# Kernel optimization log

Measured on AMD Instinct MI355X. Metric: run time of the kernel, lower is better.

## Reference

```python
import jax, jax.numpy as jnp
import numpy as np

KEYS = 11     # inference_keys: number of heatmap channels / keypoints
NSTACK = 4
B, H, W = 16, 128, 128


def setup_inputs() -> dict:
    key = jax.random.key(0)
    k1, k2, k3 = jax.random.split(key, 3)
    combined_preds = jax.random.normal(k1, (B, NSTACK, 2 * KEYS, H, W), dtype=jnp.float32)
    heatmaps = jax.random.uniform(k2, (B, KEYS, H, W), dtype=jnp.float32)
    # labels[..., 9] and [..., 10] are keypoint coords; scale to [0, 160) so some
    # fall outside [0, H)=[0,128) and exercise the validity-mask branch.
    labels = jax.random.uniform(k3, (B, KEYS, 11), dtype=jnp.float32) * 160.0
    return {"combined_preds": combined_preds, "heatmaps": heatmaps, "labels": labels}


def reference(combined_preds, heatmaps, labels):
    keys = KEYS
    hm = combined_preds[:, :, :keys]          # [B, S, K, H, W] heatmap preds
    lb = combined_preds[:, :, keys:]          # [B, S, K, H, W] label preds
    b, s, k, m, n = hm.shape                  # m = H, n = W (code uses m for both // and %)

    # HeatmapLoss per stack, vectorized over the stack dim
    heat_loss = ((hm - heatmaps[:, None]) ** 2).sum(axis=(2, 3, 4))  # [B, S]

    # LabelLoss, fully vectorized over (B, S, K)
    flat = hm.reshape(b, s, k, m * n)
    index = jnp.argmax(flat, axis=-1)         # [B, S, K]
    x = index // m                            # matches int(index / m) in original
    y = index % m
    # a[x, y] where a is the [H, W] heatmap -> flat[x * W + y]
    a_xy = jnp.take_along_axis(flat, (x * n + y)[..., None], axis=-1)[..., 0]

    pred = lb.reshape(b, s, k, -1)            # [B, S, K, H*W]
    lab = labels[:, None]                     # [B, 1, K, 11] broadcast over stacks

    gx, gy = lab[..., 9], lab[..., 10]
    valid = (gx > 0) & (gy > 0) & (gx < m) & (gy < n)

    xf = x.astype(pred.dtype)
    yf = y.astype(pred.dtype)
    xy_loss = (gx + lab[..., 7] - xf - pred[..., 7]) ** 2 \
            + (gy + lab[..., 8] - yf - pred[..., 8]) ** 2
    conf_loss = (1.0 - a_xy) ** 2
    class_loss = ((pred[..., 0:7] - lab[..., 0:7]) ** 2).sum(axis=-1)

    per_kp = jnp.where(valid, class_loss + xy_loss + conf_loss, 0.0)  # [B, S, K]
    label_loss = per_kp.sum(axis=-1)                                   # [B, S]

    return heat_loss, label_loss
```

## Files before the change

### kernel.cpp

```cpp
#include <hip/hip_runtime.h>
#include <math.h>

#define KEYS 11
#define NSTACK 4
#define NB 16
#define HH 128
#define WW 128
#define HW (HH * WW)

__global__ void kp_zero_out(float* out) {
    out[threadIdx.x] = 0.0f;
}

__global__ __launch_bounds__(256) void kp_loss_kernel(
    const float* __restrict__ cp,
    const float* __restrict__ heat,
    const float* __restrict__ lab,
    float* __restrict__ out)
{
    const int bid = blockIdx.x;
    const int k  = bid % KEYS;
    const int bs = bid / KEYS;
    const int s  = bs % NSTACK;
    const int b  = bs / NSTACK;

    const float* __restrict__ hm = cp + ((size_t)((b * NSTACK + s) * (2 * KEYS) + k)) * HW;
    const float* __restrict__ ht = heat + ((size_t)(b * KEYS + k)) * HW;

    const int tid = threadIdx.x;
    float sum  = 0.0f;
    float vmax = -INFINITY;
    int   imax = 0;

    const float4* __restrict__ hm4 = (const float4*)hm;
    const float4* __restrict__ ht4 = (const float4*)ht;

    #pragma unroll 4
    for (int i = tid; i < HW / 4; i += 256) {
        float4 a = hm4[i];
        float4 c = ht4[i];
        float d0 = a.x - c.x, d1 = a.y - c.y, d2 = a.z - c.z, d3 = a.w - c.w;
        sum += d0 * d0 + d1 * d1 + d2 * d2 + d3 * d3;
        int base = i * 4;
        if (a.x > vmax) { vmax = a.x; imax = base;     }
        if (a.y > vmax) { vmax = a.y; imax = base + 1; }
        if (a.z > vmax) { vmax = a.z; imax = base + 2; }
        if (a.w > vmax) { vmax = a.w; imax = base + 3; }
    }

    #pragma unroll
    for (int off = 32; off > 0; off >>= 1) {
        float ov = __shfl_down(vmax, off);
        int   oi = __shfl_down(imax, off);
        float os = __shfl_down(sum,  off);
        sum += os;
        if (ov > vmax || (ov == vmax && oi < imax)) { vmax = ov; imax = oi; }
    }

    __shared__ float s_sum[4];
    __shared__ float s_v[4];
    __shared__ int   s_i[4];
    const int wave = tid >> 6;
    if ((tid & 63) == 0) { s_sum[wave] = sum; s_v[wave] = vmax; s_i[wave] = imax; }
    __syncthreads();

    if (tid == 0) {
        #pragma unroll
        for (int w = 1; w < 4; w++) {
            sum += s_sum[w];
            if (s_v[w] > vmax || (s_v[w] == vmax && s_i[w] < imax)) {
                vmax = s_v[w]; imax = s_i[w];
            }
        }
        atomicAdd(&out[bs], sum);

        const float* __restrict__ lb = cp + ((size_t)((b * NSTACK + s) * (2 * KEYS) + KEYS + k)) * HW;
        const float* __restrict__ L  = lab + (size_t)(b * KEYS + k) * 11;
        float gx = L[9], gy = L[10];
        bool valid = (gx > 0.0f) && (gy > 0.0f) && (gx < (float)HH) && (gy < (float)WW);
        if (valid) {
            float xf = (float)(imax / WW);
            float yf = (float)(imax % WW);
            float dx = gx + L[7] - xf - lb[7];
            float dy = gy + L[8] - yf - lb[8];
            float loss = dx * dx + dy * dy;
            float cm = 1.0f - vmax;
            loss += cm * cm;
            #pragma unroll
            for (int j = 0; j < 7; j++) {
                float d = lb[j] - L[j];
                loss += d * d;
            }
            atomicAdd(&out[64 + bs], loss);
        }
    }
}

extern "C" void kernel_launch(void* const* d_in, const int* in_sizes, int n_in,
                              void* d_out, int out_size, void* d_ws, size_t ws_size,
                              hipStream_t stream) {
    const float* cp   = (const float*)d_in[0];
    const float* heat = (const float*)d_in[1];
    const float* lab  = (const float*)d_in[2];
    float* out = (float*)d_out;

    kp_zero_out<<<1, 128, 0, stream>>>(out);
    kp_loss_kernel<<<NB * NSTACK * KEYS, 256, 0, stream>>>(cp, heat, lab, out);
}
```

Measured before the change: 135.8 us.

## Split each heatmap slice across four blocks and reduce partials in a final kernel

Each (batch, stack, key) heatmap slice is now processed by four blocks instead of one, each covering a quarter of the pixels. Partial sums and argmax candidates go to workspace, and a single-block final kernel merges them, computes the label loss and writes outputs directly. This replaces the zeroing kernel and atomics and raises block count for more memory-level parallelism. The cost is an extra serial single-block launch with workspace round trips. Argmax tie-breaking still favours the lower chunk because the merge uses a strict greater-than in chunk order.

```diff
diff --git a/kernel.cpp b/kernel.cpp
--- a/kernel.cpp
+++ b/kernel.cpp
@@ -7,39 +7,38 @@
 #define HH 128
 #define WW 128
 #define HW (HH * WW)
+#define CHUNKS 4
+#define CHUNK_F4 1024
+#define NSLICE (NB * NSTACK * KEYS)
+#define NPART (NSLICE * CHUNKS)
 
-__global__ void kp_zero_out(float* out) {
-    out[threadIdx.x] = 0.0f;
-}
 
-__global__ __launch_bounds__(256) void kp_loss_kernel(
+__global__ __launch_bounds__(256) void kp_partial_kernel(
     const float* __restrict__ cp,
     const float* __restrict__ heat,
-    const float* __restrict__ lab,
-    float* __restrict__ out)
+    float* __restrict__ ws)
 {
-    const int bid = blockIdx.x;
-    const int k  = bid % KEYS;
-    const int bs = bid / KEYS;
-    const int s  = bs % NSTACK;
-    const int b  = bs / NSTACK;
+    const int bid   = blockIdx.x;
+    const int c     = bid & 3;
+    const int slice = bid >> 2;
+    const int k  = slice % KEYS;
+    const int bs = slice / KEYS;
+    const int b  = bs >> 2;
 
-    const float* __restrict__ hm = cp + ((size_t)((b * NSTACK + s) * (2 * KEYS) + k)) * HW;
-    const float* __restrict__ ht = heat + ((size_t)(b * KEYS + k)) * HW;
+    const float4* __restrict__ hm4 = (const float4*)(cp + ((size_t)(bs * (2 * KEYS) + k)) * HW);
+    const float4* __restrict__ ht4 = (const float4*)(heat + ((size_t)(b * KEYS + k)) * HW);
 
     const int tid = threadIdx.x;
     float sum  = 0.0f;
     float vmax = -INFINITY;
     int   imax = 0;
 
-    const float4* __restrict__ hm4 = (const float4*)hm;
-    const float4* __restrict__ ht4 = (const float4*)ht;
-
-    #pragma unroll 4
-    for (int i = tid; i < HW / 4; i += 256) {
+    #pragma unroll
+    for (int j = 0; j < 4; j++) {
+        int i = c * CHUNK_F4 + tid + j * 256;
         float4 a = hm4[i];
-        float4 c = ht4[i];
-        float d0 = a.x - c.x, d1 = a.y - c.y, d2 = a.z - c.z, d3 = a.w - c.w;
+        float4 h = ht4[i];
+        float d0 = a.x - h.x, d1 = a.y - h.y, d2 = a.z - h.z, d3 = a.w - h.w;
         sum += d0 * d0 + d1 * d1 + d2 * d2 + d3 * d3;
         int base = i * 4;
         if (a.x > vmax) { vmax = a.x; imax = base;     }
@@ -72,18 +71,51 @@
                 vmax = s_v[w]; imax = s_i[w];
             }
         }
-        atomicAdd(&out[bs], sum);
+        ws[bid]        = sum;
+        ws[4096 + bid] = vmax;
+        ((int*)ws)[8192 + bid] = imax;
+    }
+}
 
-        const float* __restrict__ lb = cp + ((size_t)((b * NSTACK + s) * (2 * KEYS) + KEYS + k)) * HW;
+__global__ __launch_bounds__(768) void kp_final_kernel(
+    const float* __restrict__ cp,
+    const float* __restrict__ lab,
+    const float* __restrict__ ws,
+    float* __restrict__ out)
+{
+    __shared__ float sh[NSLICE];
+    __shared__ float sl[NSLICE];
+
+    const int t = threadIdx.x;
+    if (t < NSLICE) {
+        const int slice = t;
+        const int k  = slice % KEYS;
+        const int bs = slice / KEYS;
+        const int b  = bs >> 2;
+
+        float sum  = 0.0f;
+        float vmax = -INFINITY;
+        int   imax = 0;
+        #pragma unroll
+        for (int c = 0; c < CHUNKS; c++) {
+            int p = slice * CHUNKS + c;
+            float v = ws[4096 + p];
+            if (v > vmax) { vmax = v; imax = ((const int*)ws)[8192 + p]; }
+            sum += ws[p];
+        }
+        sh[t] = sum;
+
         const float* __restrict__ L  = lab + (size_t)(b * KEYS + k) * 11;
         float gx = L[9], gy = L[10];
-        bool valid = (gx > 0.0f) && (gy > 0.0f) && (gx < (float)HH) && (gy < (float)WW);
-        if (valid) {
+        float loss = 0.0f;
+        if ((gx > 0.0f) && (gy > 0.0f) && (gx < (float)HH) && (gy < (float)WW)) {
+            const float* __restrict__ lb =
+                cp + ((size_t)(bs * (2 * KEYS) + KEYS + k)) * HW;
             float xf = (float)(imax / WW);
             float yf = (float)(imax % WW);
             float dx = gx + L[7] - xf - lb[7];
             float dy = gy + L[8] - yf - lb[8];
-            float loss = dx * dx + dy * dy;
+            loss = dx * dx + dy * dy;
             float cm = 1.0f - vmax;
             loss += cm * cm;
             #pragma unroll
@@ -91,8 +123,20 @@
                 float d = lb[j] - L[j];
                 loss += d * d;
             }
-            atomicAdd(&out[64 + bs], loss);
         }
+        sl[t] = loss;
+    }
+    __syncthreads();
+
+    if (t < 64) {
+        float a = 0.0f, c = 0.0f;
+        #pragma unroll
+        for (int k = 0; k < KEYS; k++) {
+            a += sh[t * KEYS + k];
+            c += sl[t * KEYS + k];
+        }
+        out[t]      = a;
+        out[64 + t] = c;
     }
 }
 
@@ -103,7 +147,8 @@
     const float* heat = (const float*)d_in[1];
     const float* lab  = (const float*)d_in[2];
     float* out = (float*)d_out;
+    float* ws  = (float*)d_ws;
 
-    kp_zero_out<<<1, 128, 0, stream>>>(out);
-    kp_loss_kernel<<<NB * NSTACK * KEYS, 256, 0, stream>>>(cp, heat, lab, out);
+    kp_partial_kernel<<<NPART, 256, 0, stream>>>(cp, heat, ws);
+    kp_final_kernel<<<1, 768, 0, stream>>>(cp, lab, ws, out);
 }
```

After: 138.0 us. Within noise of the previous version (+1.7%).
